# Kernel optimization log

Hardware: AMD Instinct MI355X
Metric: run time of the kernel (lower is better)

Reference implementation:

```python
import jax, jax.numpy as jnp
import numpy as np

N = 50000      # nodes
E = 1600000    # edges (avg degree 32)
D = 64         # in_features
OUT = 64       # out_features


def setup_inputs() -> dict:
    key = jax.random.key(0)
    ks = jax.random.split(key, 6)
    x = jax.random.normal(ks[0], (N, D), jnp.float32)
    h0 = jax.random.normal(ks[1], (N, D), jnp.float32)
    edge_row = jax.random.randint(ks[2], (E,), 0, N, jnp.int32)
    edge_col = jax.random.randint(ks[3], (E,), 0, N, jnp.int32)
    edge_vals = jax.random.uniform(ks[4], (E,), jnp.float32)  # normalized adj values
    stdv = 1.0 / np.sqrt(OUT)
    W = jax.random.uniform(ks[5], (D, OUT), jnp.float32, -stdv, stdv)
    lamda = jnp.full((1,), 0.5, jnp.float32)
    s = jnp.full((1,), 0.1, jnp.float32)  # alpha in GCNII
    l = 4  # layer index
    return {"x": x, "h0": h0, "edge_vals": edge_vals, "W": W,
            "edge_row": edge_row, "edge_col": edge_col,
            "lamda": lamda, "s": s, "l": l}


def reference(x, h0, edge_vals, W, edge_row, edge_col, lamda, s, l):
    # theta = lamda / l
    theta = lamda / jnp.float32(l)  # [1]
    # hi = spmm(adj, x): COO gather-scale-scatter
    msgs = edge_vals[:, None] * x[edge_col]            # [E, D]
    hi = jax.ops.segment_sum(msgs, edge_row, num_segments=N)  # [N, D]
    # useAOR=True, variant=False: support = (1-s)*hi + s*h0; r = support
    support = (1.0 - s) * hi + s * h0                  # [N, D]
    # useDLR=True: output = theta * support @ W + (1-theta) * support
    output = theta * (support @ W) + (1.0 - theta) * support  # [N, OUT]
    # residual=False
    return output
```

## Files before the change

kernel.cpp:

```cpp
#include <hip/hip_runtime.h>

#define NN 50000
#define NE 1600000
#define DD 64
#define RB 128
#define NBK 391
#define BINS 512
#define EPB 4096
#define NBLKA 391
#define CAP 6144
#define G4 800000
#define CONVB 196

__device__ __forceinline__ unsigned f2bf(float f) {
    unsigned u = __float_as_uint(f);
    u += 0x7FFFu + ((u >> 16) & 1u);
    return (u >> 16) & 0xFFFFu;
}

__global__ __launch_bounds__(1024) void scatter_conv(
    const int* __restrict__ erow, const int* __restrict__ ecol,
    const float* __restrict__ evals, const float* __restrict__ x,
    uint2* __restrict__ xb, int* __restrict__ gcur,
    unsigned* __restrict__ pkv, unsigned char* __restrict__ rlb)
{
    int tid = threadIdx.x;
    if (blockIdx.x >= NBLKA) {
        int t = (blockIdx.x - NBLKA) * 1024 + tid;
        const float4* x4 = reinterpret_cast<const float4*>(x);
        #pragma unroll
        for (int i = 0; i < 4; ++i) {
            int g = i * (CONVB * 1024) + t;
            if (g < G4) {
                float4 v = x4[g];
                uint2 o;
                o.x = f2bf(v.x) | (f2bf(v.y) << 16);
                o.y = f2bf(v.z) | (f2bf(v.w) << 16);
                xb[g] = o;
            }
        }
        return;
    }

    __shared__ int hist[BINS];
    __shared__ int lstart[BINS];
    __shared__ int gbase[BINS];
    __shared__ unsigned datap[EPB];
    __shared__ unsigned char datarl[EPB];
    __shared__ unsigned short sbkt[EPB];

    if (tid < BINS) hist[tid] = 0;
    __syncthreads();

    int base = blockIdx.x * EPB;
    int r[4], c[4], bk[4]; float v[4];
    #pragma unroll
    for (int i = 0; i < 4; ++i) {
        int e = base + i * 1024 + tid;
        if (e < NE) {
            r[i] = erow[e]; c[i] = ecol[e]; v[i] = evals[e];
            bk[i] = r[i] >> 7;
            atomicAdd(&hist[bk[i]], 1);
        } else bk[i] = -1;
    }
    __syncthreads();

    if (tid < 64) {
        int cc[8], s = 0;
        #pragma unroll
        for (int i = 0; i < 8; ++i) { cc[i] = hist[tid * 8 + i]; s += cc[i]; }
        int vv = s;
        #pragma unroll
        for (int off = 1; off < 64; off <<= 1) {
            int u = __shfl_up(vv, off, 64);
            if (tid >= off) vv += u;
        }
        int run = vv - s;
        #pragma unroll
        for (int i = 0; i < 8; ++i) { lstart[tid * 8 + i] = run; run += cc[i]; }
    }
    __syncthreads();

    if (tid < BINS) {
        int cnt = hist[tid];
        gbase[tid] = cnt ? atomicAdd(&gcur[tid], cnt) : 0;
        hist[tid] = lstart[tid];
    }
    __syncthreads();

    #pragma unroll
    for (int i = 0; i < 4; ++i) {
        if (bk[i] >= 0) {
            int p = atomicAdd(&hist[bk[i]], 1);
            datap[p]  = (f2bf(v[i]) << 16) | (unsigned)c[i];
            datarl[p] = (unsigned char)(r[i] & (RB - 1));
            sbkt[p]   = (unsigned short)bk[i];
        }
    }
    __syncthreads();

    int total = NE - base; if (total > EPB) total = EPB;
    #pragma unroll
    for (int i = 0; i < 4; ++i) {
        int slot = i * 1024 + tid;
        if (slot < total) {
            int bb = sbkt[slot];
            int dst = bb * CAP + gbase[bb] + slot - lstart[bb];
            pkv[dst] = datap[slot];
            rlb[dst] = datarl[slot];
        }
    }
}

__global__ __launch_bounds__(1024) void row_sort(
    const int* __restrict__ gcur, unsigned* pkv,
    const unsigned char* __restrict__ rlb, int2* __restrict__ rs)
{
    __shared__ int rhist[RB];
    __shared__ int rstart[RB + 1];

    int tid = threadIdx.x;
    int b = blockIdx.x;
    int base = b * CAP;
    int count = gcur[b];

    if (tid < RB) rhist[tid] = 0;
    __syncthreads();

    unsigned av[CAP / 1024];
    int rl[CAP / 1024];
    #pragma unroll
    for (int i = 0; i < CAP / 1024; ++i) {
        int idx = i * 1024 + tid;
        if (idx < count) {
            av[i] = pkv[base + idx];
            rl[i] = rlb[base + idx];
            atomicAdd(&rhist[rl[i]], 1);
        } else rl[i] = -1;
    }
    __syncthreads();

    if (tid < 64) {
        int c0 = rhist[tid * 2], c1 = rhist[tid * 2 + 1];
        int ssum = c0 + c1, vv = ssum;
        #pragma unroll
        for (int off = 1; off < 64; off <<= 1) {
            int u = __shfl_up(vv, off, 64);
            if (tid >= off) vv += u;
        }
        int run = vv - ssum;
        rstart[tid * 2]     = run;
        rstart[tid * 2 + 1] = run + c0;
        if (tid == 63) rstart[RB] = run + c0 + c1;
    }
    __syncthreads();

    if (tid < RB) {
        int rr = b * RB + tid;
        if (rr < NN)
            rs[rr] = make_int2(base + rstart[tid], rstart[tid + 1] - rstart[tid]);
        rhist[tid] = rstart[tid];
    }
    __syncthreads();

    int p[CAP / 1024];
    #pragma unroll
    for (int i = 0; i < CAP / 1024; ++i)
        if (rl[i] >= 0) p[i] = atomicAdd(&rhist[rl[i]], 1);
    __syncthreads();
    #pragma unroll
    for (int i = 0; i < CAP / 1024; ++i)
        if (rl[i] >= 0) pkv[base + p[i]] = av[i];
}

__global__ __launch_bounds__(256) void spmm_gemm(
    const uint2* __restrict__ xb, const float* __restrict__ h0,
    const float* __restrict__ W,  const float* __restrict__ lamda,
    const float* __restrict__ s_ptr, const int* __restrict__ l_ptr,
    const int2* __restrict__ rs, const unsigned* __restrict__ pkv,
    float* __restrict__ out)
{
    __shared__ float Wp[DD * DD];

    float theta = lamda[0] / (float)l_ptr[0];
    float s     = s_ptr[0];

    for (int i = threadIdx.x; i < DD * DD; i += 256) {
        int k = i >> 6, j = i & 63;
        float wv = theta * W[i];
        if (k == j) wv += (1.0f - theta);
        Wp[i] = wv;
    }
    __syncthreads();

    int g  = threadIdx.x >> 4;
    int f4 = threadIdx.x & 15;
    int r  = blockIdx.x * 16 + g;

    int2 se = rs[r];
    int e   = se.x;
    int end = se.x + se.y;

    float4 acc = make_float4(0.f, 0.f, 0.f, 0.f);

    #define FMA1(U, Q)                                                      \
        {                                                                   \
            float vv = __uint_as_float((U) & 0xFFFF0000u);                  \
            acc.x = fmaf(vv, __uint_as_float((Q).x << 16), acc.x);          \
            acc.y = fmaf(vv, __uint_as_float((Q).x & 0xFFFF0000u), acc.y);  \
            acc.z = fmaf(vv, __uint_as_float((Q).y << 16), acc.z);          \
            acc.w = fmaf(vv, __uint_as_float((Q).y & 0xFFFF0000u), acc.w);  \
        }

    while (e + 16 <= end) {
        unsigned u[16]; uint2 q[16];
        #pragma unroll
        for (int j = 0; j < 16; ++j) u[j] = pkv[e + j];
        #pragma unroll
        for (int j = 0; j < 16; ++j)
            q[j] = xb[(size_t)(u[j] & 0xFFFFu) * 16 + f4];
        #pragma unroll
        for (int j = 0; j < 16; ++j) FMA1(u[j], q[j]);
        e += 16;
    }
    if (e + 8 <= end) {
        unsigned u[8]; uint2 q[8];
        #pragma unroll
        for (int j = 0; j < 8; ++j) u[j] = pkv[e + j];
        #pragma unroll
        for (int j = 0; j < 8; ++j)
            q[j] = xb[(size_t)(u[j] & 0xFFFFu) * 16 + f4];
        #pragma unroll
        for (int j = 0; j < 8; ++j) FMA1(u[j], q[j]);
        e += 8;
    }
    for (; e < end; ++e) {
        unsigned u = pkv[e];
        uint2 q = xb[(size_t)(u & 0xFFFFu) * 16 + f4];
        FMA1(u, q);
    }
    #undef FMA1

    float4 hb = *reinterpret_cast<const float4*>(h0 + (size_t)r * DD + f4 * 4);
    float oms = 1.0f - s;
    float4 sup;
    sup.x = oms * acc.x + s * hb.x;
    sup.y = oms * acc.y + s * hb.y;
    sup.z = oms * acc.z + s * hb.z;
    sup.w = oms * acc.w + s * hb.w;

    float4 o = make_float4(0.f, 0.f, 0.f, 0.f);
    int lanebase = threadIdx.x & 48;
    #pragma unroll
    for (int k = 0; k < DD; ++k) {
        float comp = ((k & 3) == 0) ? sup.x :
                     ((k & 3) == 1) ? sup.y :
                     ((k & 3) == 2) ? sup.z : sup.w;
        float sk = __shfl(comp, lanebase + (k >> 2), 64);
        float4 w = *reinterpret_cast<const float4*>(&Wp[k * DD + f4 * 4]);
        o.x = fmaf(sk, w.x, o.x);
        o.y = fmaf(sk, w.y, o.y);
        o.z = fmaf(sk, w.z, o.z);
        o.w = fmaf(sk, w.w, o.w);
    }

    *reinterpret_cast<float4*>(out + (size_t)r * DD + f4 * 4) = o;
}

extern "C" void kernel_launch(void* const* d_in, const int* in_sizes, int n_in,
                              void* d_out, int out_size, void* d_ws, size_t ws_size,
                              hipStream_t stream) {
    const float* x     = (const float*)d_in[0];
    const float* h0    = (const float*)d_in[1];
    const float* evals = (const float*)d_in[2];
    const float* W     = (const float*)d_in[3];
    const int*   erow  = (const int*)d_in[4];
    const int*   ecol  = (const int*)d_in[5];
    const float* lamda = (const float*)d_in[6];
    const float* s_ptr = (const float*)d_in[7];
    const int*   l_ptr = (const int*)d_in[8];
    float* out = (float*)d_out;

    char* ws = (char*)d_ws;
    int*           gcur = (int*)ws;
    int2*          rs   = (int2*)(ws + 2048);
    size_t         pkv_off = 2048 + (((size_t)NN * 8 + 255) & ~(size_t)255);
    unsigned*      pkv  = (unsigned*)(ws + pkv_off);
    uint2*         xb   = (uint2*)(ws + pkv_off + (size_t)NBK * CAP * 4);
    unsigned char* rlb  = (unsigned char*)(ws + pkv_off + (size_t)NBK * CAP * 4
                                              + (size_t)NN * DD * 2);

    hipMemsetAsync(gcur, 0, 2048, stream);

    scatter_conv<<<NBLKA + CONVB, 1024, 0, stream>>>(erow, ecol, evals, x, xb,
                                                     gcur, pkv, rlb);
    row_sort    <<<NBK, 1024, 0, stream>>>(gcur, pkv, rlb, rs);
    spmm_gemm   <<<NN / 16, 256, 0, stream>>>(xb, h0, W, lamda, s_ptr, l_ptr,
                                              rs, pkv, out);
}
```

Measured before the change: 79.01 us.

## Pad row segments to multiples of 8 and split each row across two lane groups

The row sort now pads each row's edge segment up to a multiple of 8 with zero entries (value 0, column 0). The SpMM kernel can then drop its tail loops and use 32 lanes per row instead of 16: two 16-lane halves take alternating 8-edge chunks and the final 64x64 GEMM k-range, and shuffle-xor reductions combine the halves. This doubles the threads in flight for the latency-bound gathers and removes divergent tails, and it adds launch_bounds occupancy hints. In exchange it does wasted loads and FMAs on padding, adds extra shuffles, and padding could overflow the per-bucket CAP if buckets are dense.

After: 71.76 us. 1.1x faster.

```diff
diff --git a/kernel.cpp b/kernel.cpp
--- a/kernel.cpp
+++ b/kernel.cpp
@@ -141,8 +141,9 @@
     __syncthreads();
 
     if (tid < 64) {
-        int c0 = rhist[tid * 2], c1 = rhist[tid * 2 + 1];
-        int ssum = c0 + c1, vv = ssum;
+        int pc0 = (rhist[tid * 2] + 7) & ~7;
+        int pc1 = (rhist[tid * 2 + 1] + 7) & ~7;
+        int ssum = pc0 + pc1, vv = ssum;
         #pragma unroll
         for (int off = 1; off < 64; off <<= 1) {
             int u = __shfl_up(vv, off, 64);
@@ -150,8 +151,8 @@
         }
         int run = vv - ssum;
         rstart[tid * 2]     = run;
-        rstart[tid * 2 + 1] = run + c0;
-        if (tid == 63) rstart[RB] = run + c0 + c1;
+        rstart[tid * 2 + 1] = run + pc0;
+        if (tid == 63) rstart[RB] = run + pc0 + pc1;
     }
     __syncthreads();
 
@@ -168,12 +169,16 @@
     for (int i = 0; i < CAP / 1024; ++i)
         if (rl[i] >= 0) p[i] = atomicAdd(&rhist[rl[i]], 1);
     __syncthreads();
+
     #pragma unroll
     for (int i = 0; i < CAP / 1024; ++i)
         if (rl[i] >= 0) pkv[base + p[i]] = av[i];
-}
-
-__global__ __launch_bounds__(256) void spmm_gemm(
+    if (tid < RB)
+        for (int idx = rhist[tid]; idx < rstart[tid + 1]; ++idx)
+            pkv[base + idx] = 0;
+}
+
+__global__ __launch_bounds__(256, 4) void spmm_gemm(
     const uint2* __restrict__ xb, const float* __restrict__ h0,
     const float* __restrict__ W,  const float* __restrict__ lamda,
     const float* __restrict__ s_ptr, const int* __restrict__ l_ptr,
@@ -193,12 +198,12 @@
     }
     __syncthreads();
 
-    int g  = threadIdx.x >> 4;
-    int f4 = threadIdx.x & 15;
-    int r  = blockIdx.x * 16 + g;
+    int tid    = threadIdx.x;
+    int f4     = tid & 15;
+    int parity = (tid >> 4) & 1;
+    int r      = blockIdx.x * 8 + (tid >> 5);
 
     int2 se = rs[r];
-    int e   = se.x;
     int end = se.x + se.y;
 
     float4 acc = make_float4(0.f, 0.f, 0.f, 0.f);
@@ -212,18 +217,7 @@
             acc.w = fmaf(vv, __uint_as_float((Q).y & 0xFFFF0000u), acc.w);  \
         }
 
-    while (e + 16 <= end) {
-        unsigned u[16]; uint2 q[16];
-        #pragma unroll
-        for (int j = 0; j < 16; ++j) u[j] = pkv[e + j];
-        #pragma unroll
-        for (int j = 0; j < 16; ++j)
-            q[j] = xb[(size_t)(u[j] & 0xFFFFu) * 16 + f4];
-        #pragma unroll
-        for (int j = 0; j < 16; ++j) FMA1(u[j], q[j]);
-        e += 16;
-    }
-    if (e + 8 <= end) {
+    for (int e = se.x + parity * 8; e < end; e += 16) {
         unsigned u[8]; uint2 q[8];
         #pragma unroll
         for (int j = 0; j < 8; ++j) u[j] = pkv[e + j];
@@ -232,14 +226,13 @@
             q[j] = xb[(size_t)(u[j] & 0xFFFFu) * 16 + f4];
         #pragma unroll
         for (int j = 0; j < 8; ++j) FMA1(u[j], q[j]);
-        e += 8;
-    }
-    for (; e < end; ++e) {
-        unsigned u = pkv[e];
-        uint2 q = xb[(size_t)(u & 0xFFFFu) * 16 + f4];
-        FMA1(u, q);
     }
     #undef FMA1
+
+    acc.x += __shfl_xor(acc.x, 16, 64);
+    acc.y += __shfl_xor(acc.y, 16, 64);
+    acc.z += __shfl_xor(acc.z, 16, 64);
+    acc.w += __shfl_xor(acc.w, 16, 64);
 
     float4 hb = *reinterpret_cast<const float4*>(h0 + (size_t)r * DD + f4 * 4);
     float oms = 1.0f - s;
@@ -250,21 +243,27 @@
     sup.w = oms * acc.w + s * hb.w;
 
     float4 o = make_float4(0.f, 0.f, 0.f, 0.f);
-    int lanebase = threadIdx.x & 48;
-    #pragma unroll
-    for (int k = 0; k < DD; ++k) {
-        float comp = ((k & 3) == 0) ? sup.x :
-                     ((k & 3) == 1) ? sup.y :
-                     ((k & 3) == 2) ? sup.z : sup.w;
-        float sk = __shfl(comp, lanebase + (k >> 2), 64);
+    int lanebase = tid & 48;
+    #pragma unroll
+    for (int kk = 0; kk < 32; ++kk) {
+        int k = parity * 32 + kk;
+        float comp = ((kk & 3) == 0) ? sup.x :
+                     ((kk & 3) == 1) ? sup.y :
+                     ((kk & 3) == 2) ? sup.z : sup.w;
+        float sk = __shfl(comp, lanebase + parity * 8 + (kk >> 2), 64);
         float4 w = *reinterpret_cast<const float4*>(&Wp[k * DD + f4 * 4]);
         o.x = fmaf(sk, w.x, o.x);
         o.y = fmaf(sk, w.y, o.y);
         o.z = fmaf(sk, w.z, o.z);
         o.w = fmaf(sk, w.w, o.w);
     }
-
-    *reinterpret_cast<float4*>(out + (size_t)r * DD + f4 * 4) = o;
+    o.x += __shfl_xor(o.x, 16, 64);
+    o.y += __shfl_xor(o.y, 16, 64);
+    o.z += __shfl_xor(o.z, 16, 64);
+    o.w += __shfl_xor(o.w, 16, 64);
+
+    if (parity == 0)
+        *reinterpret_cast<float4*>(out + (size_t)r * DD + f4 * 4) = o;
 }
 
 extern "C" void kernel_launch(void* const* d_in, const int* in_sizes, int n_in,
@@ -295,6 +294,6 @@
     scatter_conv<<<NBLKA + CONVB, 1024, 0, stream>>>(erow, ecol, evals, x, xb,
                                                      gcur, pkv, rlb);
     row_sort    <<<NBK, 1024, 0, stream>>>(gcur, pkv, rlb, rs);
-    spmm_gemm   <<<NN / 16, 256, 0, stream>>>(xb, h0, W, lamda, s_ptr, l_ptr,
-                                              rs, pkv, out);
-}
+    spmm_gemm   <<<NN / 8, 256, 0, stream>>>(xb, h0, W, lamda, s_ptr, l_ptr,
+                                             rs, pkv, out);
+}
```
